# Kernel optimization log

Hardware: AMD Instinct MI355X
Metric: run time of the kernel (lower is better)

Reference implementation:

```python
import jax, jax.numpy as jnp
import numpy as np

B, T, D = 2, 2048, 1280
H = 20
DH = D // H  # 64
S_PAST = 2048


def setup_inputs() -> dict:
    key = jax.random.key(0)
    ks = jax.random.split(key, 7)
    return {
        "x": jax.random.normal(ks[0], (B, T, D), dtype=jnp.float32),
        "past_K": jax.random.normal(ks[1], (B, H, S_PAST, DH), dtype=jnp.float32),
        "past_V": jax.random.normal(ks[2], (B, H, S_PAST, DH), dtype=jnp.float32),
        "w_q": jax.random.normal(ks[3], (D, D), dtype=jnp.float32),
        "w_k": jax.random.normal(ks[4], (D, D), dtype=jnp.float32),
        "w_v": jax.random.normal(ks[5], (D, D), dtype=jnp.float32),
        "W_o": jax.random.normal(ks[6], (D, D), dtype=jnp.float32),
    }


def reference(x, past_K, past_V, w_q, w_k, w_v, W_o):
    b, t, _ = x.shape
    # projections
    q = x @ w_q  # [B,T,D]
    k = x @ w_k
    v = x @ w_v
    # split heads -> [B,H,T,DH]
    Q = q.reshape(b, t, H, DH).transpose(0, 2, 1, 3)
    K = k.reshape(b, t, H, DH).transpose(0, 2, 1, 3)
    V = v.reshape(b, t, H, DH).transpose(0, 2, 1, 3)
    # concat KV cache along sequence dim
    K = jnp.concatenate([past_K, K], axis=-2)  # [B,H,S_past+T,DH]
    V = jnp.concatenate([past_V, V], axis=-2)
    # attention (no causal mask, matching the original module)
    scores = jnp.einsum("bhtd,bhsd->bhts", Q, K) / jnp.sqrt(jnp.float32(DH))
    attn = jax.nn.softmax(scores, axis=-1)
    values = jnp.einsum("bhts,bhsd->bhtd", attn, V)  # [B,H,T,DH]
    values = values.transpose(0, 2, 1, 3).reshape(b, t, D)
    out = values @ W_o
    return out, K, V
```

## Files before the change

### kernel.cpp

```cpp
#include <hip/hip_runtime.h>

#define NB 2
#define NH 20
#define TT 2048
#define DD 1280
#define DHH 64
#define SP 2048
#define SS 4096
#define MM (NB*TT)

typedef __attribute__((ext_vector_type(8))) short bf16x8;
typedef __attribute__((ext_vector_type(4))) float f32x4;
typedef unsigned short u16;
typedef unsigned int u32;

__device__ __forceinline__ f32x4 mfma16(bf16x8 a, bf16x8 b, f32x4 c) {
  return __builtin_amdgcn_mfma_f32_16x16x32_bf16(a, b, c, 0, 0, 0);
}

__device__ __forceinline__ u16 f2bf(float f) {
  u32 x = __builtin_bit_cast(u32, f);
  x += 0x7fffu + ((x >> 16) & 1u);
  return (u16)(x >> 16);
}
__device__ __forceinline__ float bf2f(u16 u) {
  u32 x = ((u32)u) << 16;
  return __builtin_bit_cast(float, x);
}

__device__ __forceinline__ float fexp2(float x) {
#if __has_builtin(__builtin_amdgcn_exp2f)
  return __builtin_amdgcn_exp2f(x);
#else
  return exp2f(x);
#endif
}

__device__ __forceinline__ u32 cvtpk(float lo, float hi) {
  u32 r;
  asm("v_cvt_pk_bf16_f32 %0, %1, %2" : "=v"(r) : "v"(lo), "v"(hi));
  return r;
}

#define VMCNT0() asm volatile("s_waitcnt vmcnt(0)" ::: "memory")
#define BAR() __builtin_amdgcn_s_barrier()

template<int ROWS>
__device__ __forceinline__ void stage_swz(char* lds, const u16* __restrict__ gsrc,
                                          int ld, int tid) {
  constexpr int ITER = ROWS * 8 / 256;
#pragma unroll
  for (int i = 0; i < ITER; ++i) {
    int id = i * 256 + tid;
    int row = id >> 3, c = id & 7;
    int cs = c ^ (row & 7);
    const u16* src = gsrc + row * ld + cs * 8;
    __builtin_amdgcn_global_load_lds(
        (const __attribute__((address_space(1))) u32*)src,
        (__attribute__((address_space(3))) u32*)(lds + id * 16), 16, 0, 0);
  }
}

__device__ __forceinline__ void gload16(const u16* src, char* ldst) {
  __builtin_amdgcn_global_load_lds(
      (const __attribute__((address_space(1))) u32*)src,
      (__attribute__((address_space(3))) u32*)ldst, 16, 0, 0);
}

__device__ __forceinline__ bf16x8 frag_swz(const char* lds, int row, int cc) {
  return *(const bf16x8*)(lds + row * 128 + ((cc ^ (row & 7)) << 4));
}
__device__ __forceinline__ bf16x8 frag32(const char* lds, int row, int cc) {
  return *(const bf16x8*)(lds + row * 64 + ((cc ^ (row & 3)) << 4));
}

__global__ void splitx(const float* __restrict__ x, u16* __restrict__ xh,
                       u16* __restrict__ xl) {
  int i = blockIdx.x * 256 + threadIdx.x;
  float4 v = ((const float4*)x)[i];
  ushort4 hi, lo;
  hi.x = f2bf(v.x); lo.x = f2bf(v.x - bf2f(hi.x));
  hi.y = f2bf(v.y); lo.y = f2bf(v.y - bf2f(hi.y));
  hi.z = f2bf(v.z); lo.z = f2bf(v.z - bf2f(hi.z));
  hi.w = f2bf(v.w); lo.w = f2bf(v.w - bf2f(hi.w));
  ((ushort4*)xh)[i] = hi;
  ((ushort4*)xl)[i] = lo;
}

__global__ void transw(const float* __restrict__ wq, const float* __restrict__ wk,
                       const float* __restrict__ wv, const float* __restrict__ wo,
                       u16* __restrict__ wqkvh, u16* __restrict__ wqkvl,
                       u16* __restrict__ wot) {
  __shared__ float tile[64][65];
  int mat = blockIdx.z;
  const float* src = mat == 0 ? wq : mat == 1 ? wk : mat == 2 ? wv : wo;
  int k0 = blockIdx.x * 64, n0 = blockIdx.y * 64;
  int tid = threadIdx.x;
#pragma unroll
  for (int rep = 0; rep < 16; ++rep) {
    int id = rep * 256 + tid;
    int kl = id >> 6, nl = id & 63;
    tile[nl][kl] = src[(k0 + kl) * DD + n0 + nl];
  }
  __syncthreads();
#pragma unroll
  for (int rep = 0; rep < 16; ++rep) {
    int id = rep * 256 + tid;
    int nl = id >> 6, kl = id & 63;
    float v = tile[nl][kl];
    u16 hi = f2bf(v);
    if (mat < 3) {
      int idx = (mat * DD + n0 + nl) * DD + k0 + kl;
      wqkvh[idx] = hi;
      wqkvl[idx] = f2bf(v - bf2f(hi));
    } else {
      wot[(n0 + nl) * DD + k0 + kl] = hi;
    }
  }
}

__global__ void pastk(const float* __restrict__ pK, float* __restrict__ dK,
                      u16* __restrict__ Kh, u16* __restrict__ Kl) {
  int i = blockIdx.x * 256 + threadIdx.x;
  int e = i * 4;
  int dh = e & 63;
  int s = (e >> 6) & (SP - 1);
  int bh = e >> 17;
  float4 v = *(const float4*)(pK + e);
  int o = (bh * SS + s) * DHH + dh;
  *(float4*)(dK + o) = v;
  ushort4 hi, lo;
  hi.x = f2bf(v.x); lo.x = f2bf(v.x - bf2f(hi.x));
  hi.y = f2bf(v.y); lo.y = f2bf(v.y - bf2f(hi.y));
  hi.z = f2bf(v.z); lo.z = f2bf(v.z - bf2f(hi.z));
  hi.w = f2bf(v.w); lo.w = f2bf(v.w - bf2f(hi.w));
  *(ushort4*)(Kh + o) = hi;
  *(ushort4*)(Kl + o) = lo;
}

__global__ void pastv(const float* __restrict__ pV, float* __restrict__ dV,
                      u16* __restrict__ Vt) {
  __shared__ u16 tile[64][72];
  int bi = blockIdx.x;
  int bh = bi >> 5, st = bi & 31;
  int s0 = st * 64;
  int tid = threadIdx.x;
  const float* src = pV + (bh * SP + s0) * DHH;
  float* dst = dV + (bh * SS + s0) * DHH;
#pragma unroll
  for (int rep = 0; rep < 16; ++rep) {
    int id = rep * 256 + tid;
    int sl = id >> 6, dh = id & 63;
    float v = src[sl * DHH + dh];
    dst[sl * DHH + dh] = v;
    tile[dh][sl] = f2bf(v);
  }
  __syncthreads();
  u16* vdst = Vt + (bh * DHH) * SS + s0;
#pragma unroll
  for (int rep = 0; rep < 4; ++rep) {
    int id = rep * 256 + tid;
    int dh = id >> 4, s4 = (id & 15) * 4;
    ushort4 vv;
    vv.x = tile[dh][s4];     vv.y = tile[dh][s4 + 1];
    vv.z = tile[dh][s4 + 2]; vv.w = tile[dh][s4 + 3];
    *(ushort4*)(vdst + dh * SS + s4) = vv;
  }
}

__launch_bounds__(256, 2)
__global__ void gemm_qkv(const u16* __restrict__ xh, const u16* __restrict__ xl,
                         const u16* __restrict__ wh, const u16* __restrict__ wl,
                         u16* __restrict__ Qh, u16* __restrict__ Ql,
                         u16* __restrict__ Kh, u16* __restrict__ Kl,
                         u16* __restrict__ Vt,
                         float* __restrict__ dK, float* __restrict__ dV) {
  __shared__ __align__(16) char sm[65536];
  int tid = threadIdx.x, lane = tid & 63, w = tid >> 6;
  int wm = w >> 1, wn = w & 1;
  int r15 = lane & 15, grp = lane >> 4;
  int mBase = blockIdx.x * 128;
  int by = blockIdx.y;
  int nGlob = by * 128;
  const bool split = (by < 20);
  f32x4 acc[4][4] = {};
  int id0 = tid, id1 = 256 + tid;
  int r0 = id0 >> 2, c0 = id0 & 3;
  int r1 = id1 >> 2, c1 = id1 & 3;
  int so0 = r0 * DD + (c0 ^ (r0 & 3)) * 8;
  int so1 = r1 * DD + (c1 ^ (r1 & 3)) * 8;
  const u16* aH = xh + mBase * DD;
  const u16* aL = xl + mBase * DD;
  const u16* bH = wh + nGlob * DD;
  const u16* bL = wl + nGlob * DD;
  int do0 = id0 * 16, do1 = id1 * 16;

  auto stage = [&](int buf, int k0) {
    char* b = sm + buf * 32768;
    gload16(aH + k0 + so0, b + do0);
    gload16(aH + k0 + so1, b + do1);
    gload16(bH + k0 + so0, b + 16384 + do0);
    gload16(bH + k0 + so1, b + 16384 + do1);
    if (split) {
      gload16(aL + k0 + so0, b + 8192 + do0);
      gload16(aL + k0 + so1, b + 8192 + do1);
      gload16(bL + k0 + so0, b + 24576 + do0);
      gload16(bL + k0 + so1, b + 24576 + do1);
    }
  };
  auto compute = [&](int buf) {
    const char* b = sm + buf * 32768;
    bf16x8 fah[4], fal[4], fbh[4], fbl[4];
#pragma unroll
    for (int i = 0; i < 4; ++i) {
      fah[i] = frag32(b, wm * 64 + i * 16 + r15, grp);
      fbh[i] = frag32(b + 16384, wn * 64 + i * 16 + r15, grp);
      if (split) {
        fal[i] = frag32(b + 8192, wm * 64 + i * 16 + r15, grp);
        fbl[i] = frag32(b + 24576, wn * 64 + i * 16 + r15, grp);
      }
    }
    __builtin_amdgcn_s_setprio(1);
    if (split) {
#pragma unroll
      for (int i = 0; i < 4; ++i)
#pragma unroll
        for (int j = 0; j < 4; ++j) {
          acc[i][j] = mfma16(fah[i], fbh[j], acc[i][j]);
          acc[i][j] = mfma16(fah[i], fbl[j], acc[i][j]);
          acc[i][j] = mfma16(fal[i], fbh[j], acc[i][j]);
        }
    } else {
#pragma unroll
      for (int i = 0; i < 4; ++i)
#pragma unroll
        for (int j = 0; j < 4; ++j)
          acc[i][j] = mfma16(fah[i], fbh[j], acc[i][j]);
    }
    __builtin_amdgcn_s_setprio(0);
  };

  stage(0, 0);
  VMCNT0(); BAR();
#pragma unroll 2
  for (int step = 0; step < 39; ++step) {
    stage((step + 1) & 1, (step + 1) * 32);
    compute(step & 1);
    VMCNT0(); BAR();
  }
  compute(1);

  int proj = by / 10;
  int nb = (by % 10) * 128 + wn * 64;
#pragma unroll
  for (int i = 0; i < 4; ++i)
#pragma unroll
    for (int j = 0; j < 4; ++j)
#pragma unroll
      for (int r = 0; r < 4; ++r) {
        int m = mBase + wm * 64 + i * 16 + grp * 4 + r;
        int n = nb + j * 16 + r15;
        float v = acc[i][j][r];
        int b = m >> 11, t = m & 2047;
        int h = n >> 6, dh = n & 63;
        int bhh = b * NH + h;
        if (proj == 0) {
          float q = v * 0.180336880111f;
          u16 hi = f2bf(q);
          int idx = (bhh * TT + t) * DHH + dh;
          Qh[idx] = hi;
          Ql[idx] = f2bf(q - bf2f(hi));
        } else if (proj == 1) {
          int idx = (bhh * SS + SP + t) * DHH + dh;
          dK[idx] = v;
          u16 hi = f2bf(v);
          Kh[idx] = hi;
          Kl[idx] = f2bf(v - bf2f(hi));
        } else {
          int idx = (bhh * SS + SP + t) * DHH + dh;
          dV[idx] = v;
          Vt[(bhh * DHH + dh) * SS + SP + t] = f2bf(v);
        }
      }
}

__launch_bounds__(256, 2)
__global__ void attn(const u16* __restrict__ Qh, const u16* __restrict__ Ql,
                     const u16* __restrict__ Kh, const u16* __restrict__ Kl,
                     const u16* __restrict__ Vt, u16* __restrict__ ao) {
  __shared__ __align__(16) char smem[49152];
  __shared__ __align__(16) u16 Pw[4][16][72];
  __shared__ __align__(16) float bc[4][16];
  int d = blockIdx.x;
  int xcd = d & 7, sl = d >> 3;
  int bh = xcd * 5 + (sl >> 4);
  int q0 = (sl & 15) * 128;
  int tid = threadIdx.x, lane = tid & 63, w = tid >> 6;
  int r15 = lane & 15, grp = lane >> 4;
  int qbase = q0 + w * 32;
  bf16x8 fqh[2][2], fql[2][2];
#pragma unroll
  for (int qt = 0; qt < 2; ++qt) {
    int qrow = qbase + qt * 16 + r15;
    const u16* qb = Qh + (bh * TT + qrow) * DHH + grp * 8;
    const u16* qbl = Ql + (bh * TT + qrow) * DHH + grp * 8;
    fqh[qt][0] = *(const bf16x8*)qb;   fqh[qt][1] = *(const bf16x8*)(qb + 32);
    fql[qt][0] = *(const bf16x8*)qbl;  fql[qt][1] = *(const bf16x8*)(qbl + 32);
  }
  float mrun[2] = {-1e30f, -1e30f};
  float lrun[2] = {0.f, 0.f};
  f32x4 oacc[2][4] = {};
  int id0 = tid, id1 = 256 + tid;
  int r0 = id0 >> 3, c0 = id0 & 7;
  int r1 = id1 >> 3, c1 = id1 & 7;
  const u16* kh0 = Kh + bh * SS * DHH + r0 * DHH + (c0 ^ (r0 & 7)) * 8;
  const u16* kh1 = Kh + bh * SS * DHH + r1 * DHH + (c1 ^ (r1 & 7)) * 8;
  const u16* kl0 = Kl + bh * SS * DHH + r0 * DHH + (c0 ^ (r0 & 7)) * 8;
  const u16* kl1 = Kl + bh * SS * DHH + r1 * DHH + (c1 ^ (r1 & 7)) * 8;
  const u16* v0 = Vt + bh * DHH * SS + r0 * SS + (c0 ^ (r0 & 7)) * 8;
  const u16* v1 = Vt + bh * DHH * SS + r1 * SS + (c1 ^ (r1 & 7)) * 8;
  int do0 = id0 * 16, do1 = id1 * 16;

  auto stage = [&](int buf) {
    char* b = smem + buf * 24576;
    gload16(kh0, b + do0);          gload16(kh1, b + do1);
    gload16(kl0, b + 8192 + do0);   gload16(kl1, b + 8192 + do1);
    gload16(v0, b + 16384 + do0);   gload16(v1, b + 16384 + do1);
    kh0 += 64 * DHH; kh1 += 64 * DHH;
    kl0 += 64 * DHH; kl1 += 64 * DHH;
    v0 += 64; v1 += 64;
  };
  auto compute = [&](int buf) {
    const char* cb = smem + buf * 24576;
    const char* Klc = cb + 8192;
    const char* Vsc = cb + 16384;
    bf16x8 kf[4][2], klf[4][2];
#pragma unroll
    for (int kt = 0; kt < 4; ++kt)
#pragma unroll
      for (int ks = 0; ks < 2; ++ks) {
        kf[kt][ks] = frag_swz(cb, kt * 16 + r15, ks * 4 + grp);
        klf[kt][ks] = frag_swz(Klc, kt * 16 + r15, ks * 4 + grp);
      }
#pragma unroll
    for (int qt = 0; qt < 2; ++qt) {
      f32x4 st[4];
      __builtin_amdgcn_s_setprio(1);
#pragma unroll
      for (int kt = 0; kt < 4; ++kt) {
        f32x4 a = {0.f, 0.f, 0.f, 0.f};
#pragma unroll
        for (int ks = 0; ks < 2; ++ks) {
          a = mfma16(kf[kt][ks], fqh[qt][ks], a);
          a = mfma16(kf[kt][ks], fql[qt][ks], a);
          a = mfma16(klf[kt][ks], fqh[qt][ks], a);
        }
        st[kt] = a;
      }
      __builtin_amdgcn_s_setprio(0);
      float cm = fmaxf(fmaxf(fmaxf(st[0][0], st[0][1]), fmaxf(st[0][2], st[0][3])),
                       fmaxf(fmaxf(st[1][0], st[1][1]), fmaxf(st[1][2], st[1][3])));
      cm = fmaxf(cm, fmaxf(fmaxf(fmaxf(st[2][0], st[2][1]), fmaxf(st[2][2], st[2][3])),
                           fmaxf(fmaxf(st[3][0], st[3][1]), fmaxf(st[3][2], st[3][3]))));
      cm = fmaxf(cm, __shfl_xor(cm, 16));
      cm = fmaxf(cm, __shfl_xor(cm, 32));
      if (!__all(cm <= mrun[qt] + 8.f)) {
        float mnew = fmaxf(mrun[qt], cm);
        float sc = fexp2(mrun[qt] - mnew);
        lrun[qt] *= sc;
        mrun[qt] = mnew;
        if (grp == 0) bc[w][r15] = sc;
        f32x4 scv = *(const f32x4*)&bc[w][grp * 4];
#pragma unroll
        for (int dd = 0; dd < 4; ++dd) {
          oacc[qt][dd][0] *= scv[0]; oacc[qt][dd][1] *= scv[1];
          oacc[qt][dd][2] *= scv[2]; oacc[qt][dd][3] *= scv[3];
        }
      }
      float m = mrun[qt];
      float ps = 0.f;
#pragma unroll
      for (int kt = 0; kt < 4; ++kt)
#pragma unroll
        for (int r = 0; r < 4; ++r) {
          float p = fexp2(st[kt][r] - m);
          st[kt][r] = p;
          ps += p;
        }
      ps += __shfl_xor(ps, 16);
      ps += __shfl_xor(ps, 32);
      lrun[qt] += ps;
#pragma unroll
      for (int kt = 0; kt < 4; ++kt) {
        u32 w0 = cvtpk(st[kt][0], st[kt][1]);
        u32 w1 = cvtpk(st[kt][2], st[kt][3]);
        uint2 pk = {w0, w1};
        *(uint2*)&Pw[w][r15][kt * 16 + grp * 4] = pk;
      }
      bf16x8 pa0 = *(const bf16x8*)&Pw[w][r15][grp * 8];
      bf16x8 pa1 = *(const bf16x8*)&Pw[w][r15][32 + grp * 8];
      __builtin_amdgcn_s_setprio(1);
#pragma unroll
      for (int dd = 0; dd < 4; ++dd) {
        bf16x8 vf0 = frag_swz(Vsc, dd * 16 + r15, grp);
        bf16x8 vf1 = frag_swz(Vsc, dd * 16 + r15, 4 + grp);
        oacc[qt][dd] = mfma16(pa0, vf0, oacc[qt][dd]);
        oacc[qt][dd] = mfma16(pa1, vf1, oacc[qt][dd]);
      }
      __builtin_amdgcn_s_setprio(0);
    }
  };

  stage(0);
  VMCNT0(); BAR();
#pragma unroll 2
  for (int it = 0; it < SS / 64 - 1; ++it) {
    stage((it + 1) & 1);
    compute(it & 1);
    VMCNT0(); BAR();
  }
  compute(1);

  int b = bh / NH, h = bh % NH;
#pragma unroll
  for (int qt = 0; qt < 2; ++qt) {
    float inv = 1.0f / lrun[qt];
    if (grp == 0) bc[w][r15] = inv;
    f32x4 li = *(const f32x4*)&bc[w][grp * 4];
#pragma unroll
    for (int dd = 0; dd < 4; ++dd)
#pragma unroll
      for (int r = 0; r < 4; ++r) {
        int q = qbase + qt * 16 + grp * 4 + r;
        int col = h * DHH + dd * 16 + r15;
        ao[(b * TT + q) * DD + col] = f2bf(oacc[qt][dd][r] * li[r]);
      }
  }
}

__launch_bounds__(256, 2)
__global__ void gemm_out(const u16* __restrict__ ao, const u16* __restrict__ wot,
                         float* __restrict__ out) {
  __shared__ __align__(16) char sm[32768];
  char* As = sm;
  char* Bs = sm + 16384;
  int tid = threadIdx.x, lane = tid & 63, w = tid >> 6;
  int wm = w >> 1, wn = w & 1;
  int r15 = lane & 15, grp = lane >> 4;
  int mBase = blockIdx.x * 128, nBase = blockIdx.y * 128;
  f32x4 acc[4][4] = {};
  for (int k0 = 0; k0 < DD; k0 += 64) {
    stage_swz<128>(As, ao + mBase * DD + k0, DD, tid);
    stage_swz<128>(Bs, wot + nBase * DD + k0, DD, tid);
    __syncthreads();
#pragma unroll
    for (int kk = 0; kk < 2; ++kk) {
      int cc = kk * 4 + grp;
      bf16x8 fa[4], fb[4];
#pragma unroll
      for (int i = 0; i < 4; ++i) {
        fa[i] = frag_swz(As, wm * 64 + i * 16 + r15, cc);
        fb[i] = frag_swz(Bs, wn * 64 + i * 16 + r15, cc);
      }
#pragma unroll
      for (int i = 0; i < 4; ++i)
#pragma unroll
        for (int j = 0; j < 4; ++j)
          acc[i][j] = mfma16(fa[i], fb[j], acc[i][j]);
    }
    __syncthreads();
  }
#pragma unroll
  for (int i = 0; i < 4; ++i)
#pragma unroll
    for (int j = 0; j < 4; ++j)
#pragma unroll
      for (int r = 0; r < 4; ++r) {
        int m = mBase + wm * 64 + i * 16 + grp * 4 + r;
        int n = nBase + wn * 64 + j * 16 + r15;
        out[m * DD + n] = acc[i][j][r];
      }
}

extern "C" void kernel_launch(void* const* d_in, const int* in_sizes, int n_in,
                              void* d_out, int out_size, void* d_ws, size_t ws_size,
                              hipStream_t stream) {
  const float* x  = (const float*)d_in[0];
  const float* pK = (const float*)d_in[1];
  const float* pV = (const float*)d_in[2];
  const float* wq = (const float*)d_in[3];
  const float* wk = (const float*)d_in[4];
  const float* wv = (const float*)d_in[5];
  const float* wo = (const float*)d_in[6];

  float* out = (float*)d_out;
  float* dK  = out + NB * TT * DD;
  float* dV  = dK + NB * NH * SS * DHH;

  u16* xh    = (u16*)d_ws;
  u16* xl    = xh + MM * DD;
  u16* wqkvh = xl + MM * DD;
  u16* wqkvl = wqkvh + 3 * DD * DD;
  u16* wot   = wqkvl + 3 * DD * DD;
  u16* Qh    = wot + DD * DD;
  u16* Ql    = Qh + MM * DD;
  u16* Kh    = Ql + MM * DD;
  u16* Kl    = Kh + NB * NH * SS * DHH;
  u16* Vt    = Kl + NB * NH * SS * DHH;
  u16* ao    = xh;

  splitx<<<dim3(MM * DD / 4 / 256), 256, 0, stream>>>(x, xh, xl);
  transw<<<dim3(20, 20, 4), 256, 0, stream>>>(wq, wk, wv, wo, wqkvh, wqkvl, wot);
  pastk<<<dim3(NB * NH * SP * DHH / 4 / 256), 256, 0, stream>>>(pK, dK, Kh, Kl);
  pastv<<<dim3(NB * NH * (SP / 64)), 256, 0, stream>>>(pV, dV, Vt);
  gemm_qkv<<<dim3(32, 30), 256, 0, stream>>>(xh, xl, wqkvh, wqkvl,
                                             Qh, Ql, Kh, Kl, Vt, dK, dV);
  attn<<<dim3(NB * NH * (TT / 128)), 256, 0, stream>>>(Qh, Ql, Kh, Kl, Vt, ao);
  gemm_out<<<dim3(32, 10), 256, 0, stream>>>(ao, wot, out);
}
```

Baseline: 437.3 us.

## Single-buffer attention K/V staging to raise occupancy to three blocks per CU

Replaces the double-buffered 48KB LDS staging in the attention kernel with single 24KB buffers and raises launch bounds to 3 blocks per CU. The loop now loads a tile, synchronises, computes and synchronises again, so global loads no longer overlap compute within a block; the extra resident blocks are meant to hide that latency instead. It also interleaves the two query tiles so each K/V fragment is read from LDS once and reused across both, with a per-tile P buffer. The risk is exposed load latency, two barriers per iteration, and register pressure under the tighter launch bound.

```diff
diff --git a/kernel.cpp b/kernel.cpp
--- a/kernel.cpp
+++ b/kernel.cpp
@@ -284,12 +284,14 @@
       }
 }
 
-__launch_bounds__(256, 2)
+__launch_bounds__(256, 3)
 __global__ void attn(const u16* __restrict__ Qh, const u16* __restrict__ Ql,
                      const u16* __restrict__ Kh, const u16* __restrict__ Kl,
                      const u16* __restrict__ Vt, u16* __restrict__ ao) {
-  __shared__ __align__(16) char smem[49152];
-  __shared__ __align__(16) u16 Pw[4][16][72];
+  __shared__ __align__(16) char Ks[8192];
+  __shared__ __align__(16) char Kls[8192];
+  __shared__ __align__(16) char Vs[8192];
+  __shared__ __align__(16) u16 Pw[4][2][16][72];
   __shared__ __align__(16) float bc[4][16];
   int d = blockIdx.x;
   int xcd = d & 7, sl = d >> 3;
@@ -319,49 +321,47 @@
   const u16* kl1 = Kl + bh * SS * DHH + r1 * DHH + (c1 ^ (r1 & 7)) * 8;
   const u16* v0 = Vt + bh * DHH * SS + r0 * SS + (c0 ^ (r0 & 7)) * 8;
   const u16* v1 = Vt + bh * DHH * SS + r1 * SS + (c1 ^ (r1 & 7)) * 8;
-  int do0 = id0 * 16, do1 = id1 * 16;
-
-  auto stage = [&](int buf) {
-    char* b = smem + buf * 24576;
-    gload16(kh0, b + do0);          gload16(kh1, b + do1);
-    gload16(kl0, b + 8192 + do0);   gload16(kl1, b + 8192 + do1);
-    gload16(v0, b + 16384 + do0);   gload16(v1, b + 16384 + do1);
+  char* dK0 = Ks + id0 * 16;  char* dK1 = Ks + id1 * 16;
+  char* dL0 = Kls + id0 * 16; char* dL1 = Kls + id1 * 16;
+  char* dV0 = Vs + id0 * 16;  char* dV1 = Vs + id1 * 16;
+
+  for (int it = 0; it < SS / 64; ++it) {
+    gload16(kh0, dK0); gload16(kh1, dK1);
+    gload16(kl0, dL0); gload16(kl1, dL1);
+    gload16(v0, dV0);  gload16(v1, dV1);
     kh0 += 64 * DHH; kh1 += 64 * DHH;
     kl0 += 64 * DHH; kl1 += 64 * DHH;
     v0 += 64; v1 += 64;
-  };
-  auto compute = [&](int buf) {
-    const char* cb = smem + buf * 24576;
-    const char* Klc = cb + 8192;
-    const char* Vsc = cb + 16384;
-    bf16x8 kf[4][2], klf[4][2];
-#pragma unroll
-    for (int kt = 0; kt < 4; ++kt)
-#pragma unroll
-      for (int ks = 0; ks < 2; ++ks) {
-        kf[kt][ks] = frag_swz(cb, kt * 16 + r15, ks * 4 + grp);
-        klf[kt][ks] = frag_swz(Klc, kt * 16 + r15, ks * 4 + grp);
-      }
+    __syncthreads();
+    f32x4 st[2][4];
+    __builtin_amdgcn_s_setprio(1);
+#pragma unroll
+    for (int kt = 0; kt < 4; ++kt) {
+      bf16x8 k0f = frag_swz(Ks, kt * 16 + r15, grp);
+      bf16x8 k1f = frag_swz(Ks, kt * 16 + r15, 4 + grp);
+      bf16x8 l0f = frag_swz(Kls, kt * 16 + r15, grp);
+      bf16x8 l1f = frag_swz(Kls, kt * 16 + r15, 4 + grp);
+#pragma unroll
+      for (int qt = 0; qt < 2; ++qt) {
+        f32x4 a = {0.f, 0.f, 0.f, 0.f};
+        a = mfma16(k0f, fqh[qt][0], a);
+        a = mfma16(k0f, fql[qt][0], a);
+        a = mfma16(l0f, fqh[qt][0], a);
+        a = mfma16(k1f, fqh[qt][1], a);
+        a = mfma16(k1f, fql[qt][1], a);
+        a = mfma16(l1f, fqh[qt][1], a);
+        st[qt][kt] = a;
+      }
+    }
+    __builtin_amdgcn_s_setprio(0);
 #pragma unroll
     for (int qt = 0; qt < 2; ++qt) {
-      f32x4 st[4];
-      __builtin_amdgcn_s_setprio(1);
-#pragma unroll
-      for (int kt = 0; kt < 4; ++kt) {
-        f32x4 a = {0.f, 0.f, 0.f, 0.f};
-#pragma unroll
-        for (int ks = 0; ks < 2; ++ks) {
-          a = mfma16(kf[kt][ks], fqh[qt][ks], a);
-          a = mfma16(kf[kt][ks], fql[qt][ks], a);
-          a = mfma16(klf[kt][ks], fqh[qt][ks], a);
-        }
-        st[kt] = a;
-      }
-      __builtin_amdgcn_s_setprio(0);
-      float cm = fmaxf(fmaxf(fmaxf(st[0][0], st[0][1]), fmaxf(st[0][2], st[0][3])),
-                       fmaxf(fmaxf(st[1][0], st[1][1]), fmaxf(st[1][2], st[1][3])));
-      cm = fmaxf(cm, fmaxf(fmaxf(fmaxf(st[2][0], st[2][1]), fmaxf(st[2][2], st[2][3])),
-                           fmaxf(fmaxf(st[3][0], st[3][1]), fmaxf(st[3][2], st[3][3]))));
+      float cm = fmaxf(
+          fmaxf(fmaxf(st[qt][0][0], st[qt][0][1]), fmaxf(st[qt][0][2], st[qt][0][3])),
+          fmaxf(fmaxf(st[qt][1][0], st[qt][1][1]), fmaxf(st[qt][1][2], st[qt][1][3])));
+      cm = fmaxf(cm, fmaxf(
+          fmaxf(fmaxf(st[qt][2][0], st[qt][2][1]), fmaxf(st[qt][2][2], st[qt][2][3])),
+          fmaxf(fmaxf(st[qt][3][0], st[qt][3][1]), fmaxf(st[qt][3][2], st[qt][3][3]))));
       cm = fmaxf(cm, __shfl_xor(cm, 16));
       cm = fmaxf(cm, __shfl_xor(cm, 32));
       if (!__all(cm <= mrun[qt] + 8.f)) {
@@ -383,8 +383,8 @@
       for (int kt = 0; kt < 4; ++kt)
 #pragma unroll
         for (int r = 0; r < 4; ++r) {
-          float p = fexp2(st[kt][r] - m);
-          st[kt][r] = p;
+          float p = fexp2(st[qt][kt][r] - m);
+          st[qt][kt][r] = p;
           ps += p;
         }
       ps += __shfl_xor(ps, 16);
@@ -392,35 +392,32 @@
       lrun[qt] += ps;
 #pragma unroll
       for (int kt = 0; kt < 4; ++kt) {
-        u32 w0 = cvtpk(st[kt][0], st[kt][1]);
-        u32 w1 = cvtpk(st[kt][2], st[kt][3]);
+        u32 w0 = cvtpk(st[qt][kt][0], st[qt][kt][1]);
+        u32 w1 = cvtpk(st[qt][kt][2], st[qt][kt][3]);
         uint2 pk = {w0, w1};
-        *(uint2*)&Pw[w][r15][kt * 16 + grp * 4] = pk;
-      }
-      bf16x8 pa0 = *(const bf16x8*)&Pw[w][r15][grp * 8];
-      bf16x8 pa1 = *(const bf16x8*)&Pw[w][r15][32 + grp * 8];
-      __builtin_amdgcn_s_setprio(1);
-#pragma unroll
-      for (int dd = 0; dd < 4; ++dd) {
-        bf16x8 vf0 = frag_swz(Vsc, dd * 16 + r15, grp);
-        bf16x8 vf1 = frag_swz(Vsc, dd * 16 + r15, 4 + grp);
-        oacc[qt][dd] = mfma16(pa0, vf0, oacc[qt][dd]);
-        oacc[qt][dd] = mfma16(pa1, vf1, oacc[qt][dd]);
-      }
-      __builtin_amdgcn_s_setprio(0);
-    }
-  };
-
-  stage(0);
-  VMCNT0(); BAR();
-#pragma unroll 2
-  for (int it = 0; it < SS / 64 - 1; ++it) {
-    stage((it + 1) & 1);
-    compute(it & 1);
-    VMCNT0(); BAR();
-  }
-  compute(1);
-
+        *(uint2*)&Pw[w][qt][r15][kt * 16 + grp * 4] = pk;
+      }
+    }
+    bf16x8 pa[2][2];
+#pragma unroll
+    for (int qt = 0; qt < 2; ++qt) {
+      pa[qt][0] = *(const bf16x8*)&Pw[w][qt][r15][grp * 8];
+      pa[qt][1] = *(const bf16x8*)&Pw[w][qt][r15][32 + grp * 8];
+    }
+    __builtin_amdgcn_s_setprio(1);
+#pragma unroll
+    for (int dd = 0; dd < 4; ++dd) {
+      bf16x8 vf0 = frag_swz(Vs, dd * 16 + r15, grp);
+      bf16x8 vf1 = frag_swz(Vs, dd * 16 + r15, 4 + grp);
+#pragma unroll
+      for (int qt = 0; qt < 2; ++qt) {
+        oacc[qt][dd] = mfma16(pa[qt][0], vf0, oacc[qt][dd]);
+        oacc[qt][dd] = mfma16(pa[qt][1], vf1, oacc[qt][dd]);
+      }
+    }
+    __builtin_amdgcn_s_setprio(0);
+    __syncthreads();
+  }
   int b = bh / NH, h = bh % NH;
 #pragma unroll
   for (int qt = 0; qt < 2; ++qt) {
```

New measurement: 382.2 us. 12.6% less time.
